# Optimization experiments

Measured on AMD Instinct MI355X. Metric: run time of the kernel, lower is better.

## Reference

```python
import jax, jax.numpy as jnp
import numpy as np

B, N, IN_DIM, OUT_DIM, H = 8, 1024, 256, 256, 8
D = OUT_DIM // H  # head_dim = 32
NEG_INF = -1.0e9


def setup_inputs() -> dict:
    key = jax.random.key(0)
    k_x, k_adj, k_W, k_a = jax.random.split(key, 4)
    x = jax.random.normal(k_x, (B, N, IN_DIM), dtype=jnp.float32)
    adj = jax.random.randint(k_adj, (B, N, N), 0, 2, dtype=jnp.int32)
    # nn.Linear(in_dim, out_dim, bias=False): weight [out_dim, in_dim]
    lim = 1.0 / np.sqrt(IN_DIM)
    W = jax.random.uniform(k_W, (OUT_DIM, IN_DIM), jnp.float32, -lim, lim)
    # a: (1, H, 2*D), xavier_uniform with gain=1.414
    gain = 1.414
    bound = gain * np.sqrt(6.0 / (H + 2 * D))
    a = jax.random.uniform(k_a, (1, H, 2 * D), jnp.float32, -bound, bound)
    return {"x": x, "adj": adj, "W": W, "a": a}


def reference(x, adj, W, a):
    Bn, Nn, _ = x.shape
    h = jnp.einsum('bni,oi->bno', x, W).reshape(Bn, Nn, H, D)  # [B,N,H,D]
    # sum(cat(h_i, h_j) * a) = h_i . a_src + h_j . a_dst  (avoids O(N^2*2D) concat)
    a_src = a[0, :, :D]   # [H,D] multiplies h_i (query/row index i)
    a_dst = a[0, :, D:]   # [H,D] multiplies h_j (key/col index j)
    s_i = jnp.einsum('bnhd,hd->bnh', h, a_src)  # [B,N,H]
    s_j = jnp.einsum('bnhd,hd->bnh', h, a_dst)  # [B,N,H]
    e = s_i[:, :, None, :] + s_j[:, None, :, :]  # [B,i,j,H]
    e = jnp.where(e > 0, e, 0.2 * e)  # LeakyReLU(0.2)
    mask = (adj != 0)[..., None]      # [B,N,N,1] broadcast over heads
    e = jnp.where(mask, e, NEG_INF)
    alpha = jax.nn.softmax(e, axis=2)  # softmax over j (neighbors)
    # dropout p=0.0 -> identity
    h_prime = jnp.einsum('bijh,bjhd->bihd', alpha, h)
    h_prime = h_prime.reshape(Bn, Nn, H * D)
    return jax.nn.elu(h_prime)
```

## Files before the change

### kernel.cpp

```cpp
#include <hip/hip_runtime.h>
#include <cmath>

namespace {
constexpr int B = 8, N = 1024, IND = 256, OUTD = 256, H = 8, D = 32;
constexpr float LOG2E = 1.4426950408889634f;
}

typedef __attribute__((ext_vector_type(8))) short short8v;
typedef __attribute__((ext_vector_type(4))) float f32x4;

union pk8_t {
  uint u[4];
  short8v s;
};

__device__ inline uint cvt_pk(float lo, float hi) {
  uint r;
  asm("v_cvt_pk_bf16_f32 %0, %1, %2" : "=v"(r) : "v"(lo), "v"(hi));
  return r;
}
__device__ inline float lo16f(uint u) { return __uint_as_float(u << 16); }
__device__ inline float hi16f(uint u) { return __uint_as_float(u & 0xFFFF0000u); }

__global__ __launch_bounds__(256) void gat_k1(
    const float* __restrict__ x, const float* __restrict__ W,
    const float* __restrict__ a, const int* __restrict__ adj,
    uint* __restrict__ bitsT, float* __restrict__ siT,
    float* __restrict__ sjT, ushort* __restrict__ hTbF) {
  const int bid = blockIdx.x;
  const int t = threadIdx.x;

  if (bid >= 512) {
    const int lane = t & 63, w = t >> 6;
    const int wid = (bid - 512) * 4 + w;
    const int b = wid >> 10, i = wid & 1023;
    const int4* ap = (const int4*)(adj + ((size_t)b * N + i) * N);
#pragma unroll
    for (int c = 0; c < 4; ++c) {
      const int4 v = ap[c * 64 + lane];
      uint val = (v.x != 0 ? 1u : 0u) | (v.y != 0 ? 2u : 0u) |
                 (v.z != 0 ? 4u : 0u) | (v.w != 0 ? 8u : 0u);
      val <<= (lane & 7) * 4;
      val |= (uint)__shfl_xor((int)val, 1);
      val |= (uint)__shfl_xor((int)val, 2);
      val |= (uint)__shfl_xor((int)val, 4);
      if ((lane & 7) == 0) {
        const int jt = c * 8 + (lane >> 3);
        bitsT[((size_t)b * 32 + jt) * N + i] = val;
      }
    }
    return;
  }

  __shared__ __align__(16) char smem[17664];
  float(*xs)[36] = (float(*)[36])smem;
  ushort* wsh = (ushort*)(smem + 9216);
  ushort* wsl = (ushort*)(smem + 13312);
  float(*tile2)[65] = (float(*)[65])smem;

  const int lane = t & 63, w = t >> 6;
  const int la = lane & 15, g = lane >> 4;
  const int work = ((bid & 7) << 6) + (bid >> 3);
  const int bx = work >> 2, by = work & 3;

  f32x4 z = {0.f, 0.f, 0.f, 0.f};
  f32x4 acc[4] = {z, z, z, z};

  const float* xp = x + (size_t)(bx * 64 + (t >> 2)) * IND + (t & 3) * 8;
  const int w_c = by * 64 + (t >> 6) * 16 + (t & 15);
  const int w_k0 = ((t >> 4) & 3) * 8;
  const float* wp = W + (size_t)w_c * IND + w_k0;

  for (int kb = 0; kb < 8; ++kb) {
    __syncthreads();
    {
      float4 v0 = *(const float4*)(xp + kb * 32);
      float4 v1 = *(const float4*)(xp + kb * 32 + 4);
      float* dst = &xs[t >> 2][(t & 3) * 8];
      *(float4*)dst = v0;
      *(float4*)(dst + 4) = v1;
    }
    {
      float4 v0 = *(const float4*)(wp + kb * 32);
      float4 v1 = *(const float4*)(wp + kb * 32 + 4);
      const float wf[8] = {v0.x, v0.y, v0.z, v0.w, v1.x, v1.y, v1.z, v1.w};
      pk8_t ph_, pl_;
#pragma unroll
      for (int p = 0; p < 4; ++p) {
        const uint hu = cvt_pk(wf[2 * p], wf[2 * p + 1]);
        ph_.u[p] = hu;
        pl_.u[p] = cvt_pk(wf[2 * p] - lo16f(hu), wf[2 * p + 1] - hi16f(hu));
      }
      *(short8v*)&wsh[t * 8] = ph_.s;
      *(short8v*)&wsl[t * 8] = pl_.s;
    }
    __syncthreads();

    const float* xr = &xs[w * 16 + la][g * 8];
    float4 u0 = *(const float4*)(xr);
    float4 u1 = *(const float4*)(xr + 4);
    const float af[8] = {u0.x, u0.y, u0.z, u0.w, u1.x, u1.y, u1.z, u1.w};
    short8v ah, al;
    {
      pk8_t ph_, pl_;
#pragma unroll
      for (int p = 0; p < 4; ++p) {
        const uint hu = cvt_pk(af[2 * p], af[2 * p + 1]);
        ph_.u[p] = hu;
        pl_.u[p] = cvt_pk(af[2 * p] - lo16f(hu), af[2 * p + 1] - hi16f(hu));
      }
      ah = ph_.s;
      al = pl_.s;
    }
#pragma unroll
    for (int ct = 0; ct < 4; ++ct) {
      const short8v bh = *(const short8v*)&wsh[ct * 512 + lane * 8];
      const short8v bl = *(const short8v*)&wsl[ct * 512 + lane * 8];
      acc[ct] = __builtin_amdgcn_mfma_f32_16x16x32_bf16(ah, bh, acc[ct], 0, 0, 0);
      acc[ct] = __builtin_amdgcn_mfma_f32_16x16x32_bf16(al, bh, acc[ct], 0, 0, 0);
      acc[ct] = __builtin_amdgcn_mfma_f32_16x16x32_bf16(ah, bl, acc[ct], 0, 0, 0);
    }
  }

  const int batch = bx >> 4;
  const int nbase = (bx & 15) * 64 + w * 16;

#pragma unroll
  for (int hp2 = 0; hp2 < 2; ++hp2) {
    const int head = by * 2 + hp2;
    const float a0 = a[head * 64 + la] * LOG2E;
    const float a1 = a[head * 64 + 16 + la] * LOG2E;
    const float a2 = a[head * 64 + 32 + la] * LOG2E;
    const float a3 = a[head * 64 + 48 + la] * LOG2E;
    float s1v[4], s2v[4];
#pragma unroll
    for (int q = 0; q < 4; ++q) {
      s1v[q] = acc[hp2 * 2][q] * a0 + acc[hp2 * 2 + 1][q] * a1;
      s2v[q] = acc[hp2 * 2][q] * a2 + acc[hp2 * 2 + 1][q] * a3;
    }
#pragma unroll
    for (int mask = 1; mask <= 8; mask <<= 1)
#pragma unroll
      for (int q = 0; q < 4; ++q) {
        s1v[q] += __shfl_xor(s1v[q], mask);
        s2v[q] += __shfl_xor(s2v[q], mask);
      }
    if (la == 0) {
#pragma unroll
      for (int q = 0; q < 4; ++q) {
        const size_t o = (size_t)(batch * H + head) * N + nbase + g * 4 + q;
        siT[o] = s1v[q];
        sjT[o] = s2v[q];
      }
    }
  }

  __syncthreads();
#pragma unroll
  for (int ct = 0; ct < 4; ++ct)
#pragma unroll
    for (int q = 0; q < 4; ++q)
      tile2[w * 16 + g * 4 + q][ct * 16 + la] = acc[ct][q];
  __syncthreads();

  const int jt0 = (bx & 15) * 2;
#pragma unroll
  for (int s = 0; s < 2; ++s) {
    const int gg = t * 2 + s;
    const int head = gg >> 8, rem = gg & 255;
    const int jt_loc = rem >> 7, half = (rem >> 6) & 1, l = rem & 63;
    const int d = half * 16 + (l & 15);
    pk8_t pk_;
#pragma unroll
    for (int p = 0; p < 4; ++p)
      pk_.u[p] = cvt_pk(tile2[jt_loc * 32 + (l >> 4) * 8 + 2 * p][head * 32 + d],
                        tile2[jt_loc * 32 + (l >> 4) * 8 + 2 * p + 1][head * 32 + d]);
    const int bh_g = batch * H + by * 2 + head;
    *(short8v*)(hTbF + ((size_t)(bh_g * 32 + jt0 + jt_loc) * 64 + l) * 16 + half * 8) = pk_.s;
  }
}

__global__ __launch_bounds__(256) void gat_agg(
    const uint* __restrict__ bitsT, const float* __restrict__ siT,
    const float* __restrict__ sjT, const ushort* __restrict__ hTbF,
    float* __restrict__ out) {
  __shared__ float sj_lds[1024];
  __shared__ uint bits_lds[32][32];
  __shared__ float part[2][64][13];
  const int t = threadIdx.x;
  const int lane = t & 63, w = t >> 6;
  const int iw = w & 1, jq = w >> 1;
  const int bid = blockIdx.x;
  const int work = ((bid & 7) << 8) + (bid >> 3);
  const int bh = work >> 5;
  const int itg = work & 31;
  const int b = bh >> 3, hh = bh & 7;
  const int i0 = itg * 32 + iw * 16;
  const int la = lane & 15, g = lane >> 4;
  const int iA = i0 + la;

  const float si_r = siT[(size_t)bh * N + iA];

  {
    float4 v = *(const float4*)(sjT + (size_t)bh * N + t * 4);
    *(float4*)&sj_lds[t * 4] = v;
    const int jt = t >> 3, c4 = (t & 7) * 4;
    uint4 bv = *(const uint4*)(bitsT + ((size_t)b * 32 + jt) * N + itg * 32 + c4);
    *(uint4*)&bits_lds[jt][c4] = bv;
  }
  __syncthreads();

  const ushort* hp = hTbF + (size_t)bh * 32768 + (size_t)jq * 16384 + lane * 16;
  const uint* blp = &bits_lds[jq * 16][iw * 16 + la];
  const float* slp = &sj_lds[jq * 512 + g * 8];

  f32x4 acc0 = {0.f, 0.f, 0.f, 0.f}, acc1 = {0.f, 0.f, 0.f, 0.f};
  f32x4 accl = {0.f, 0.f, 0.f, 0.f};
  short8v ones;
#pragma unroll
  for (int e = 0; e < 8; ++e) ones[e] = (short)0x3F80;

  uint bits_A, bits_B;
  float4 sj0A, sj1A, sj0B, sj1B;
  short8v h0A, h1A, h0B, h1B;

#define AGG_LDS(S, JT)                                     \
  bits_##S = blp[(JT)*32];                                 \
  sj0##S = *(const float4*)(slp + (JT) * 32);              \
  sj1##S = *(const float4*)(slp + (JT) * 32 + 4);

#define AGG_LOAD_H(S, JT)                                  \
  h0##S = *(const short8v*)(hp + (size_t)(JT)*1024);       \
  h1##S = *(const short8v*)(hp + (size_t)(JT)*1024 + 8);

#define AGG_COMP(S)                                                           \
  {                                                                           \
    const uint byte_ = (bits_##S >> (g * 8)) & 0xffu;                         \
    const float sjv[8] = {sj0##S.x, sj0##S.y, sj0##S.z, sj0##S.w,             \
                          sj1##S.x, sj1##S.y, sj1##S.z, sj1##S.w};            \
    float wv[8];                                                              \
    _Pragma("unroll") for (int e = 0; e < 8; ++e) {                           \
      float s = si_r + sjv[e];                                                \
      s = fmaxf(s, 0.2f * s);                                                 \
      s = ((byte_ >> e) & 1u) ? s : -INFINITY;                                \
      wv[e] = __builtin_amdgcn_exp2f(s);                                      \
    }                                                                         \
    pk8_t pk_;                                                                \
    pk_.u[0] = cvt_pk(wv[0], wv[1]);                                          \
    pk_.u[1] = cvt_pk(wv[2], wv[3]);                                          \
    pk_.u[2] = cvt_pk(wv[4], wv[5]);                                          \
    pk_.u[3] = cvt_pk(wv[6], wv[7]);                                          \
    const short8v af = pk_.s;                                                 \
    __builtin_amdgcn_s_setprio(1);                                            \
    acc0 = __builtin_amdgcn_mfma_f32_16x16x32_bf16(af, h0##S, acc0, 0, 0, 0); \
    acc1 = __builtin_amdgcn_mfma_f32_16x16x32_bf16(af, h1##S, acc1, 0, 0, 0); \
    accl = __builtin_amdgcn_mfma_f32_16x16x32_bf16(af, ones, accl, 0, 0, 0);  \
    __builtin_amdgcn_s_setprio(0);                                            \
  }

  AGG_LDS(A, 0)
  AGG_LOAD_H(A, 0)
  AGG_LDS(B, 1)
  AGG_LOAD_H(B, 1)
#pragma unroll
  for (int jt = 0; jt < 16; jt += 2) {
    AGG_COMP(A)
    if (jt + 2 < 16) { AGG_LDS(A, jt + 2) AGG_LOAD_H(A, jt + 2) }
    AGG_COMP(B)
    if (jt + 3 < 16) { AGG_LDS(B, jt + 3) AGG_LOAD_H(B, jt + 3) }
  }
#undef AGG_LDS
#undef AGG_LOAD_H
#undef AGG_COMP

  if (jq == 1) {
    float* p = part[iw][lane];
#pragma unroll
    for (int k = 0; k < 4; ++k) {
      p[k] = acc0[k];
      p[4 + k] = acc1[k];
      p[8 + k] = accl[k];
    }
  }
  __syncthreads();
  if (jq == 0) {
    const float* p = part[iw][lane];
#pragma unroll
    for (int k = 0; k < 4; ++k) {
      acc0[k] += p[k];
      acc1[k] += p[4 + k];
      accl[k] += p[8 + k];
    }
    float* op = out + ((size_t)(b * N + i0)) * OUTD + hh * D;
#pragma unroll
    for (int r = 0; r < 4; ++r) {
      const int ic = g * 4 + r;
      const float li = accl[r];
      float v0 = acc0[r] / li;
      v0 = v0 > 0.f ? v0 : expm1f(v0);
      op[(size_t)ic * OUTD + la] = v0;
      float v1 = acc1[r] / li;
      v1 = v1 > 0.f ? v1 : expm1f(v1);
      op[(size_t)ic * OUTD + 16 + la] = v1;
    }
  }
}

extern "C" void kernel_launch(void* const* d_in, const int* in_sizes, int n_in,
                              void* d_out, int out_size, void* d_ws, size_t ws_size,
                              hipStream_t stream) {
  const float* x = (const float*)d_in[0];
  const int* adj = (const int*)d_in[1];
  const float* W = (const float*)d_in[2];
  const float* a = (const float*)d_in[3];
  float* out = (float*)d_out;

  float* ws = (float*)d_ws;
  float* siT = ws;
  float* sjT = siT + (size_t)B * N * H;
  uint* bitsT = (uint*)(sjT + (size_t)B * N * H);
  ushort* hTbF = (ushort*)(bitsT + (size_t)B * 32 * N);

  gat_k1<<<512 + 2048, 256, 0, stream>>>(x, W, a, adj, bitsT, siT, sjT, hTbF);
  gat_agg<<<2048, 256, 0, stream>>>(bitsT, siT, sjT, hTbF, out);
}
```

Before: 41.29 us.

## Factor exp of LeakyReLU score into precomputed per-row and per-column exponentials

Since exp2(leaky(si+sj)) splits into exp2(si)*exp2(sj) or exp2(0.2si)*exp2(0.2sj) depending on the sign of si+sj, the first kernel now also stores -sj, exp2(sj) and exp2(0.2*sj), and the aggregation kernel replaces each per-element exp with a compare, two selects and a multiply. This removes transcendental work from the inner loop. The cost is three LDS arrays instead of one, more LDS reads per tile, and more workspace traffic. The loop also drops the LDS double-buffering and the setprio hints around the MFMAs. Skipping the max subtraction could overflow for large scores.

```diff
diff --git a/kernel.cpp b/kernel.cpp
--- a/kernel.cpp
+++ b/kernel.cpp
@@ -26,7 +26,8 @@
     const float* __restrict__ x, const float* __restrict__ W,
     const float* __restrict__ a, const int* __restrict__ adj,
     uint* __restrict__ bitsT, float* __restrict__ siT,
-    float* __restrict__ sjT, ushort* __restrict__ hTbF) {
+    float* __restrict__ nsjT, float* __restrict__ e1T,
+    float* __restrict__ e2T, ushort* __restrict__ hTbF) {
   const int bid = blockIdx.x;
   const int t = threadIdx.x;
 
@@ -150,7 +151,9 @@
       for (int q = 0; q < 4; ++q) {
         const size_t o = (size_t)(batch * H + head) * N + nbase + g * 4 + q;
         siT[o] = s1v[q];
-        sjT[o] = s2v[q];
+        nsjT[o] = -s2v[q];
+        e1T[o] = __builtin_amdgcn_exp2f(s2v[q]);
+        e2T[o] = __builtin_amdgcn_exp2f(0.2f * s2v[q]);
       }
     }
   }
@@ -182,9 +185,12 @@
 
 __global__ __launch_bounds__(256) void gat_agg(
     const uint* __restrict__ bitsT, const float* __restrict__ siT,
-    const float* __restrict__ sjT, const ushort* __restrict__ hTbF,
+    const float* __restrict__ nsjT, const float* __restrict__ e1T,
+    const float* __restrict__ e2T, const ushort* __restrict__ hTbF,
     float* __restrict__ out) {
-  __shared__ float sj_lds[1024];
+  __shared__ float nsj_lds[1024];
+  __shared__ float e1_lds[1024];
+  __shared__ float e2_lds[1024];
   __shared__ uint bits_lds[32][32];
   __shared__ float part[2][64][13];
   const int t = threadIdx.x;
@@ -200,10 +206,13 @@
   const int iA = i0 + la;
 
   const float si_r = siT[(size_t)bh * N + iA];
+  const float E1i = __builtin_amdgcn_exp2f(si_r);
+  const float E2i = __builtin_amdgcn_exp2f(0.2f * si_r);
 
   {
-    float4 v = *(const float4*)(sjT + (size_t)bh * N + t * 4);
-    *(float4*)&sj_lds[t * 4] = v;
+    *(float4*)&nsj_lds[t * 4] = *(const float4*)(nsjT + (size_t)bh * N + t * 4);
+    *(float4*)&e1_lds[t * 4] = *(const float4*)(e1T + (size_t)bh * N + t * 4);
+    *(float4*)&e2_lds[t * 4] = *(const float4*)(e2T + (size_t)bh * N + t * 4);
     const int jt = t >> 3, c4 = (t & 7) * 4;
     uint4 bv = *(const uint4*)(bitsT + ((size_t)b * 32 + jt) * N + itg * 32 + c4);
     *(uint4*)&bits_lds[jt][c4] = bv;
@@ -212,7 +221,9 @@
 
   const ushort* hp = hTbF + (size_t)bh * 32768 + (size_t)jq * 16384 + lane * 16;
   const uint* blp = &bits_lds[jq * 16][iw * 16 + la];
-  const float* slp = &sj_lds[jq * 512 + g * 8];
+  const float* nsp = &nsj_lds[jq * 512 + g * 8];
+  const float* e1p = &e1_lds[jq * 512 + g * 8];
+  const float* e2p = &e2_lds[jq * 512 + g * 8];
 
   f32x4 acc0 = {0.f, 0.f, 0.f, 0.f}, acc1 = {0.f, 0.f, 0.f, 0.f};
   f32x4 accl = {0.f, 0.f, 0.f, 0.f};
@@ -220,30 +231,31 @@
 #pragma unroll
   for (int e = 0; e < 8; ++e) ones[e] = (short)0x3F80;
 
-  uint bits_A, bits_B;
-  float4 sj0A, sj1A, sj0B, sj1B;
   short8v h0A, h1A, h0B, h1B;
 
-#define AGG_LDS(S, JT)                                     \
-  bits_##S = blp[(JT)*32];                                 \
-  sj0##S = *(const float4*)(slp + (JT) * 32);              \
-  sj1##S = *(const float4*)(slp + (JT) * 32 + 4);
-
-#define AGG_LOAD_H(S, JT)                                  \
+#define LDH(S, JT)                                         \
   h0##S = *(const short8v*)(hp + (size_t)(JT)*1024);       \
   h1##S = *(const short8v*)(hp + (size_t)(JT)*1024 + 8);
 
-#define AGG_COMP(S)                                                           \
+#define COMP(S, JT)                                                           \
   {                                                                           \
-    const uint byte_ = (bits_##S >> (g * 8)) & 0xffu;                         \
-    const float sjv[8] = {sj0##S.x, sj0##S.y, sj0##S.z, sj0##S.w,             \
-                          sj1##S.x, sj1##S.y, sj1##S.z, sj1##S.w};            \
+    const uint byte_ = (blp[(JT)*32] >> (g * 8)) & 0xffu;                     \
+    const float4 n0 = *(const float4*)(nsp + (JT) * 32);                      \
+    const float4 n1 = *(const float4*)(nsp + (JT) * 32 + 4);                  \
+    const float4 p0 = *(const float4*)(e1p + (JT) * 32);                      \
+    const float4 p1 = *(const float4*)(e1p + (JT) * 32 + 4);                  \
+    const float4 q0 = *(const float4*)(e2p + (JT) * 32);                      \
+    const float4 q1 = *(const float4*)(e2p + (JT) * 32 + 4);                  \
+    const float nv[8] = {n0.x, n0.y, n0.z, n0.w, n1.x, n1.y, n1.z, n1.w};     \
+    const float av[8] = {p0.x, p0.y, p0.z, p0.w, p1.x, p1.y, p1.z, p1.w};     \
+    const float bv[8] = {q0.x, q0.y, q0.z, q0.w, q1.x, q1.y, q1.z, q1.w};     \
     float wv[8];                                                              \
     _Pragma("unroll") for (int e = 0; e < 8; ++e) {                           \
-      float s = si_r + sjv[e];                                                \
-      s = fmaxf(s, 0.2f * s);                                                 \
-      s = ((byte_ >> e) & 1u) ? s : -INFINITY;                                \
-      wv[e] = __builtin_amdgcn_exp2f(s);                                      \
+      const bool cond = si_r > nv[e];                                         \
+      const float ea = cond ? E1i : E2i;                                      \
+      const float ej = cond ? av[e] : bv[e];                                  \
+      float wgt = ea * ej;                                                    \
+      wv[e] = ((byte_ >> e) & 1u) ? wgt : 0.f;                                \
     }                                                                         \
     pk8_t pk_;                                                                \
     pk_.u[0] = cvt_pk(wv[0], wv[1]);                                          \
@@ -251,27 +263,22 @@
     pk_.u[2] = cvt_pk(wv[4], wv[5]);                                          \
     pk_.u[3] = cvt_pk(wv[6], wv[7]);                                          \
     const short8v af = pk_.s;                                                 \
-    __builtin_amdgcn_s_setprio(1);                                            \
     acc0 = __builtin_amdgcn_mfma_f32_16x16x32_bf16(af, h0##S, acc0, 0, 0, 0); \
     acc1 = __builtin_amdgcn_mfma_f32_16x16x32_bf16(af, h1##S, acc1, 0, 0, 0); \
     accl = __builtin_amdgcn_mfma_f32_16x16x32_bf16(af, ones, accl, 0, 0, 0);  \
-    __builtin_amdgcn_s_setprio(0);                                            \
-  }
-
-  AGG_LDS(A, 0)
-  AGG_LOAD_H(A, 0)
-  AGG_LDS(B, 1)
-  AGG_LOAD_H(B, 1)
+  }
+
+  LDH(A, 0)
+  LDH(B, 1)
 #pragma unroll
   for (int jt = 0; jt < 16; jt += 2) {
-    AGG_COMP(A)
-    if (jt + 2 < 16) { AGG_LDS(A, jt + 2) AGG_LOAD_H(A, jt + 2) }
-    AGG_COMP(B)
-    if (jt + 3 < 16) { AGG_LDS(B, jt + 3) AGG_LOAD_H(B, jt + 3) }
-  }
-#undef AGG_LDS
-#undef AGG_LOAD_H
-#undef AGG_COMP
+    COMP(A, jt)
+    if (jt + 2 < 16) { LDH(A, jt + 2) }
+    COMP(B, jt + 1)
+    if (jt + 3 < 16) { LDH(B, jt + 3) }
+  }
+#undef LDH
+#undef COMP
 
   if (jq == 1) {
     float* p = part[iw][lane];
@@ -317,10 +324,13 @@
 
   float* ws = (float*)d_ws;
   float* siT = ws;
-  float* sjT = siT + (size_t)B * N * H;
-  uint* bitsT = (uint*)(sjT + (size_t)B * N * H);
+  float* nsjT = siT + (size_t)B * N * H;
+  float* e1T = nsjT + (size_t)B * N * H;
+  float* e2T = e1T + (size_t)B * N * H;
+  uint* bitsT = (uint*)(e2T + (size_t)B * N * H);
   ushort* hTbF = (ushort*)(bitsT + (size_t)B * 32 * N);
 
-  gat_k1<<<512 + 2048, 256, 0, stream>>>(x, W, a, adj, bitsT, siT, sjT, hTbF);
-  gat_agg<<<2048, 256, 0, stream>>>(bitsT, siT, sjT, hTbF, out);
-}
+  gat_k1<<<512 + 2048, 256, 0, stream>>>(x, W, a, adj, bitsT, siT, nsjT, e1T,
+                                         e2T, hTbF);
+  gat_agg<<<2048, 256, 0, stream>>>(bitsT, siT, nsjT, e1T, e2T, hTbF, out);
+}
```

New measurement: 41.31 us. No clear change (+0.0%).
